# Performance work log

Measured on AMD Instinct MI355X. Metric: run time of the kernel, lower is better.

## Reference

```python
import jax, jax.numpy as jnp
import numpy as np

H = 256      # hidden_units
NB = 2       # num_blocks
NH = 4       # num_heads
E = 8        # num_experts
K = 2        # top_k
L = 200      # maxlen
B = 128      # batch
ITEM = 100000
USER = 50000


def _ln(x, w, b, eps):
    m = x.mean(-1, keepdims=True)
    v = ((x - m) ** 2).mean(-1, keepdims=True)
    return (x - m) / jnp.sqrt(v + eps) * w + b


def setup_inputs() -> dict:
    key = jax.random.key(0)
    ks = iter(jax.random.split(key, 48))

    def n(shape, s=0.02):
        return jax.random.normal(next(ks), shape, jnp.float32) * s

    item_emb = n((ITEM + 1, H)).at[0].set(0.0)   # padding_idx=0
    pos_emb = n((L + 1, H)).at[0].set(0.0)
    user_emb = n((USER + 1, H)).at[0].set(0.0)
    return dict(
        user_ids=jax.random.randint(next(ks), (B,), 1, USER + 1),
        log_seqs=jax.random.randint(next(ks), (B, L), 0, ITEM + 1),
        item_ids=jax.random.randint(next(ks), (B,), 1, ITEM + 1),
        item_emb=item_emb, pos_emb=pos_emb, user_emb=user_emb,
        ln1_w=jnp.ones((NB, H)), ln1_b=jnp.zeros((NB, H)),
        inproj_w=n((NB, 3 * H, H)), inproj_b=jnp.zeros((NB, 3 * H)),
        outproj_w=n((NB, H, H)), outproj_b=jnp.zeros((NB, H)),
        ln2_w=jnp.ones((NB, H)), ln2_b=jnp.zeros((NB, H)),
        gate_w=n((NB, E, H)), gate_b=jnp.zeros((NB, E)),
        e_w1=n((NB, E, H, H)), e_b1=jnp.zeros((NB, E, H)),
        e_w2=n((NB, E, H, H)), e_b2=jnp.zeros((NB, E, H)),
        moeln_w=jnp.ones((NB, H)), moeln_b=jnp.zeros((NB, H)),
        lastln_w=jnp.ones((H,)), lastln_b=jnp.zeros((H,)),
    )


def reference(user_ids, log_seqs, item_ids, item_emb, pos_emb, user_emb,
              ln1_w, ln1_b, inproj_w, inproj_b, outproj_w, outproj_b,
              ln2_w, ln2_b, gate_w, gate_b, e_w1, e_b1, e_w2, e_b2,
              moeln_w, moeln_b, lastln_w, lastln_b):
    hd = H // NH
    # embeddings (padding id 0 -> zero rows)
    x = item_emb[log_seqs] * jnp.sqrt(jnp.float32(H))          # [B,L,H]
    poss = jnp.arange(1, L + 1)[None, :] * (log_seqs != 0)      # 0 where padded
    x = x + pos_emb[poss]
    causal = jnp.tril(jnp.ones((L, L), bool))

    for i in range(NB):
        # pre-LN query, raw x as key/value (matches original)
        q_in = _ln(x, ln1_w[i], ln1_b[i], 1e-8)
        wq, wk, wv = jnp.split(inproj_w[i], 3, axis=0)
        bq, bk, bv = jnp.split(inproj_b[i], 3)
        q = (q_in @ wq.T + bq).reshape(B, L, NH, hd)
        k = (x @ wk.T + bk).reshape(B, L, NH, hd)
        v = (x @ wv.T + bv).reshape(B, L, NH, hd)
        s = jnp.einsum('bqnd,bknd->bnqk', q, k) / jnp.sqrt(jnp.float32(hd))
        s = jnp.where(causal, s, -jnp.inf)
        a = jax.nn.softmax(s, axis=-1)
        ctx = jnp.einsum('bnqk,bknd->bqnd', a, v).reshape(B, L, H)
        mha = ctx @ outproj_w[i].T + outproj_b[i]
        x = q_in + mha
        x = _ln(x, ln2_w[i], ln2_b[i], 1e-8)

        # SparseMoE: top-k gate, all-expert dense compute, masked combine
        gl = jnp.einsum('bsh,eh->bse', x, gate_w[i]) + gate_b[i]
        w, idx = jax.lax.top_k(gl, K)
        w = jax.nn.softmax(w, axis=-1)
        comb = (jax.nn.one_hot(idx, E) * w[..., None]).sum(-2)   # [B,L,E]
        h = jax.nn.relu(jnp.einsum('bsh,ehd->besd', x, e_w1[i])
                        + e_b1[i][None, :, None, :])              # [B,E,L,H]
        y = jnp.einsum('besd,edh->besh', h, e_w2[i]) + e_b2[i][None, :, None, :]
        moe = jnp.einsum('bse,besh->bsh', comb, y)
        x = _ln(x + moe, moeln_w[i], moeln_b[i], 1e-5)

    x = _ln(x, lastln_w, lastln_b, 1e-8)
    final = x[:, -1, :] + user_emb[user_ids]
    return (final * item_emb[item_ids]).sum(-1)   # [B] logits
```

## Files before the change

### kernel.cpp

```cpp
#include <hip/hip_runtime.h>
#include <math.h>

#define H 256
#define NHEAD 4
#define HD 64
#define NEXP 8
#define SEQL 200
#define BATCH 128
#define NF (BATCH*SEQL)
#define KT 64
#define QT 64
#define QW 8

typedef __bf16 bf16x8 __attribute__((ext_vector_type(8)));
typedef float  f32x4  __attribute__((ext_vector_type(4)));

__device__ __forceinline__ void split8(const float* __restrict__ p, bf16x8& hi, bf16x8& lo, bool valid) {
    if (valid) {
        float4 a = *(const float4*)p;
        float4 b = *(const float4*)(p + 4);
        float x[8] = {a.x,a.y,a.z,a.w,b.x,b.y,b.z,b.w};
        #pragma unroll
        for (int j = 0; j < 8; ++j) {
            __bf16 h = (__bf16)x[j];
            hi[j] = h;
            lo[j] = (__bf16)(x[j] - (float)h);
        }
    } else {
        #pragma unroll
        for (int j = 0; j < 8; ++j) { hi[j] = (__bf16)0.f; lo[j] = (__bf16)0.f; }
    }
}

#define MFMA3(AH,AL,BH,BL,ACC) \
    ACC = __builtin_amdgcn_mfma_f32_16x16x32_bf16(AH, BH, ACC, 0, 0, 0); \
    ACC = __builtin_amdgcn_mfma_f32_16x16x32_bf16(AH, BL, ACC, 0, 0, 0); \
    ACC = __builtin_amdgcn_mfma_f32_16x16x32_bf16(AL, BH, ACC, 0, 0, 0);

__device__ __forceinline__ float blk_sum256(float v, float* s4) {
    #pragma unroll
    for (int o = 32; o > 0; o >>= 1) v += __shfl_xor(v, o, 64);
    __syncthreads();
    if ((threadIdx.x & 63) == 0) s4[threadIdx.x >> 6] = v;
    __syncthreads();
    return s4[0] + s4[1] + s4[2] + s4[3];
}

__global__ __launch_bounds__(256) void split_plain(
    const float* __restrict__ in, __bf16* __restrict__ hi, __bf16* __restrict__ lo, int n)
{
    for (int i = blockIdx.x * 256 + threadIdx.x; i < n; i += gridDim.x * 256) {
        float x = in[i];
        __bf16 h = (__bf16)x;
        hi[i] = h;
        lo[i] = (__bf16)(x - (float)h);
    }
}

__global__ __launch_bounds__(256) void split_trans(
    const float* __restrict__ in, __bf16* __restrict__ hi, __bf16* __restrict__ lo, int nmats)
{
    int n = nmats * H * H;
    for (int i = blockIdx.x * 256 + threadIdx.x; i < n; i += gridDim.x * 256) {
        int m = i / (H*H), rem = i % (H*H);
        int nn = rem / H, k = rem % H;
        float x = in[(size_t)m*H*H + (size_t)k*H + nn];
        __bf16 h = (__bf16)x;
        hi[i] = h;
        lo[i] = (__bf16)(x - (float)h);
    }
}

__global__ __launch_bounds__(256) void embed_ln_kernel(
    const int* __restrict__ seqs, const float* __restrict__ item_emb,
    const float* __restrict__ pos_emb, float* __restrict__ x,
    float* __restrict__ xln, const float* __restrict__ w, const float* __restrict__ b)
{
    __shared__ float s4[4];
    int n = blockIdx.x, t = threadIdx.x;
    int id = seqs[n];
    int pos = (id != 0) ? (n % SEQL) + 1 : 0;
    float v = item_emb[(size_t)id*H + t] * 16.0f + pos_emb[(size_t)pos*H + t];
    x[(size_t)n*H + t] = v;
    float mean = blk_sum256(v, s4) * (1.f/H);
    float d = v - mean;
    float var = blk_sum256(d*d, s4) * (1.f/H);
    xln[(size_t)n*H + t] = d * rsqrtf(var + 1e-8f) * w[t] + b[t];
}

__global__ __launch_bounds__(256) void ln_kernel(
    const float* __restrict__ in, const float* __restrict__ res,
    float* __restrict__ out, const float* __restrict__ w, const float* __restrict__ b,
    float eps, int base, int step)
{
    __shared__ float s4[4];
    int r = blockIdx.x, t = threadIdx.x;
    float v = in[(size_t)(base + r*step)*H + t];
    if (res) v += res[(size_t)r*H + t];
    float mean = blk_sum256(v, s4) * (1.f/H);
    float d = v - mean;
    float var = blk_sum256(d*d, s4) * (1.f/H);
    out[(size_t)r*H + t] = d * rsqrtf(var + eps) * w[t] + b[t];
}

__global__ __launch_bounds__(256) void ln2_gate_kernel(
    const float* __restrict__ in, const float* __restrict__ res,
    float* __restrict__ out, const float* __restrict__ w, const float* __restrict__ b,
    const float* __restrict__ gw, const float* __restrict__ gb,
    int* __restrict__ top_idx, float* __restrict__ top_w)
{
    __shared__ float s4[4];
    __shared__ float xs[H];
    __shared__ float gl[NEXP];
    int n = blockIdx.x, t = threadIdx.x;
    float v = in[(size_t)n*H + t] + res[(size_t)n*H + t];
    float mean = blk_sum256(v, s4) * (1.f/H);
    float d = v - mean;
    float var = blk_sum256(d*d, s4) * (1.f/H);
    float r = d * rsqrtf(var + 1e-8f) * w[t] + b[t];
    out[(size_t)n*H + t] = r;
    xs[t] = r;
    __syncthreads();
    int wv = t >> 6, lane = t & 63;
    float xv[4];
    #pragma unroll
    for (int c = 0; c < 4; ++c) xv[c] = xs[lane + (c<<6)];
    #pragma unroll
    for (int s = 0; s < 2; ++s) {
        int e = wv*2 + s;
        float acc = 0.f;
        #pragma unroll
        for (int c = 0; c < 4; ++c) acc += xv[c] * gw[(size_t)e*H + lane + (c<<6)];
        #pragma unroll
        for (int o = 32; o > 0; o >>= 1) acc += __shfl_xor(acc, o, 64);
        if (lane == 0) gl[e] = acc + gb[e];
    }
    __syncthreads();
    if (t == 0) {
        int i0 = 0;
        for (int e = 1; e < NEXP; ++e) if (gl[e] > gl[i0]) i0 = e;
        int i1 = -1;
        for (int e = 0; e < NEXP; ++e) { if (e == i0) continue; if (i1 < 0 || gl[e] > gl[i1]) i1 = e; }
        float e1 = expf(gl[i1] - gl[i0]);
        float w0 = 1.f / (1.f + e1);
        top_idx[n*2+0] = i0; top_idx[n*2+1] = i1;
        top_w[n*2+0] = w0;  top_w[n*2+1] = 1.f - w0;
    }
}

__global__ __launch_bounds__(256) void moe_ln_kernel(
    const float* __restrict__ x, const float* __restrict__ ybuf,
    const int* __restrict__ tok_pair, const float* __restrict__ top_w,
    float* __restrict__ out, const float* __restrict__ w, const float* __restrict__ b,
    float eps)
{
    __shared__ float s4[4];
    int r = blockIdx.x, t = threadIdx.x;
    int p0 = tok_pair[r*2], p1 = tok_pair[r*2+1];
    float v = x[(size_t)r*H + t]
            + top_w[r*2+0] * ybuf[(size_t)p0*H + t]
            + top_w[r*2+1] * ybuf[(size_t)p1*H + t];
    float mean = blk_sum256(v, s4) * (1.f/H);
    float d = v - mean;
    float var = blk_sum256(d*d, s4) * (1.f/H);
    out[(size_t)r*H + t] = d * rsqrtf(var + eps) * w[t] + b[t];
}

__global__ __launch_bounds__(256) void gemm_nt(
    const float* __restrict__ A, const float* __restrict__ W,
    const float* __restrict__ bias, float* __restrict__ out, int nrows)
{
    __shared__ float As[16][68];
    __shared__ float Ws[16][68];
    int r0 = blockIdx.x * 64;
    if (r0 >= nrows) return;
    int c0 = blockIdx.y * 64;
    int tid = threadIdx.x;
    int tx = tid & 15, ty = tid >> 4;
    int lrow = tid >> 2, lkg = (tid & 3) << 2;
    float acc[4][4] = {};
    for (int kk = 0; kk < H; kk += 16) {
        float4 av = make_float4(0.f,0.f,0.f,0.f);
        int gr = r0 + lrow;
        if (gr < nrows) av = *(const float4*)(A + (size_t)gr*H + kk + lkg);
        As[lkg+0][lrow]=av.x; As[lkg+1][lrow]=av.y; As[lkg+2][lrow]=av.z; As[lkg+3][lrow]=av.w;
        float4 wv = *(const float4*)(W + (size_t)(c0+lrow)*H + kk + lkg);
        Ws[lkg+0][lrow]=wv.x; Ws[lkg+1][lrow]=wv.y; Ws[lkg+2][lrow]=wv.z; Ws[lkg+3][lrow]=wv.w;
        __syncthreads();
        #pragma unroll
        for (int k = 0; k < 16; ++k) {
            float4 a = *(const float4*)&As[k][ty<<2];
            float4 bv = *(const float4*)&Ws[k][tx<<2];
            float aa[4] = {a.x,a.y,a.z,a.w};
            float bb[4] = {bv.x,bv.y,bv.z,bv.w};
            #pragma unroll
            for (int ii = 0; ii < 4; ++ii)
                #pragma unroll
                for (int jj = 0; jj < 4; ++jj)
                    acc[ii][jj] += aa[ii] * bb[jj];
        }
        __syncthreads();
    }
    #pragma unroll
    for (int ii = 0; ii < 4; ++ii) {
        int gr = r0 + (ty<<2) + ii;
        if (gr < nrows) {
            #pragma unroll
            for (int jj = 0; jj < 4; ++jj) {
                int gc = c0 + (tx<<2) + jj;
                out[(size_t)gr*H + gc] = acc[ii][jj] + bias[gc];
            }
        }
    }
}

template<int GATHER, int RELU>
__device__ __forceinline__ void mfma64_body(
    const float* __restrict__ A, const __bf16* __restrict__ Whi, const __bf16* __restrict__ Wlo,
    const float* __restrict__ bias, float* __restrict__ out, int nrows,
    const int* __restrict__ pair_tok)
{
    int r0 = blockIdx.x * 64;
    if (r0 >= nrows) return;
    int tid = threadIdx.x;
    int wid = tid >> 6, lane = tid & 63;
    int wm = wid >> 1, wn = wid & 1;
    int rbase = r0 + wm*32;
    int lr = lane & 15, lk = (lane >> 4) << 3;
    f32x4 acc[4][2][2] = {};
    int ar0 = rbase + lr, ar1 = ar0 + 16;
    bool v0 = ar0 < nrows, v1 = ar1 < nrows;
    int ga0 = ar0, ga1 = ar1;
    if (GATHER) { ga0 = v0 ? pair_tok[ar0] : 0; ga1 = v1 ? pair_tok[ar1] : 0; }
    const float* ap0 = A + (size_t)(v0 ? ga0 : 0)*H + lk;
    const float* ap1 = A + (size_t)(v1 ? ga1 : 0)*H + lk;
    size_t woff = (size_t)(wn*32 + lr)*H + lk;
    #pragma unroll
    for (int kk = 0; kk < H; kk += 32) {
        bf16x8 ah0, al0, ah1, al1;
        split8(ap0 + kk, ah0, al0, v0);
        split8(ap1 + kk, ah1, al1, v1);
        #pragma unroll
        for (int ct = 0; ct < 4; ++ct) {
            size_t wo = woff + (size_t)ct*64*H + kk;
            bf16x8 bh0 = *(const bf16x8*)(Whi + wo);
            bf16x8 bl0 = *(const bf16x8*)(Wlo + wo);
            bf16x8 bh1 = *(const bf16x8*)(Whi + wo + (size_t)16*H);
            bf16x8 bl1 = *(const bf16x8*)(Wlo + wo + (size_t)16*H);
            MFMA3(ah0, al0, bh0, bl0, acc[ct][0][0]);
            MFMA3(ah0, al0, bh1, bl1, acc[ct][0][1]);
            MFMA3(ah1, al1, bh0, bl0, acc[ct][1][0]);
            MFMA3(ah1, al1, bh1, bl1, acc[ct][1][1]);
        }
    }
    int lro = (lane >> 4) << 2;
    #pragma unroll
    for (int ct = 0; ct < 4; ++ct)
        #pragma unroll
        for (int mi = 0; mi < 2; ++mi)
            #pragma unroll
            for (int ni = 0; ni < 2; ++ni)
                #pragma unroll
                for (int j = 0; j < 4; ++j) {
                    int row = rbase + mi*16 + lro + j;
                    int col = ct*64 + wn*32 + ni*16 + lr;
                    if (row < nrows) {
                        float o = acc[ct][mi][ni][j] + bias[col];
                        if (RELU) o = fmaxf(o, 0.f);
                        out[(size_t)row*H + col] = o;
                    }
                }
}

__global__ __launch_bounds__(256) void mfma_z(
    const float* __restrict__ A0, const float* __restrict__ A1,
    const __bf16* __restrict__ Whi, const __bf16* __restrict__ Wlo,
    const float* __restrict__ biasbase, float* __restrict__ outbase, int nrows)
{
    int z = blockIdx.z;
    const float* A = (z == 0) ? A0 : A1;
    mfma64_body<0,0>(A, Whi + (size_t)z*H*H, Wlo + (size_t)z*H*H,
                     biasbase + (size_t)z*H, outbase + (size_t)z*NF*H, nrows, nullptr);
}

__global__ __launch_bounds__(256) void mfma_moe1(
    const float* __restrict__ X, const __bf16* __restrict__ Whi, const __bf16* __restrict__ Wlo,
    const float* __restrict__ b1base, const int* __restrict__ pair_tok,
    const int* __restrict__ offsets, const int* __restrict__ counts,
    float* __restrict__ hbuf)
{
    int e = blockIdx.z;
    int cnt = counts[e], off = offsets[e];
    mfma64_body<1,1>(X, Whi + (size_t)e*H*H, Wlo + (size_t)e*H*H,
                     b1base + (size_t)e*H, hbuf + (size_t)off*H, cnt, pair_tok + off);
}

__global__ __launch_bounds__(256) void mfma_moe2(
    const float* __restrict__ Hbuf, const __bf16* __restrict__ Whi, const __bf16* __restrict__ Wlo,
    const float* __restrict__ b2base, const int* __restrict__ offsets,
    const int* __restrict__ counts, float* __restrict__ ybuf)
{
    int e = blockIdx.z;
    int cnt = counts[e], off = offsets[e];
    mfma64_body<0,0>(Hbuf + (size_t)off*H, Whi + (size_t)e*H*H, Wlo + (size_t)e*H*H,
                     b2base + (size_t)e*H, ybuf + (size_t)off*H, cnt, nullptr);
}

__global__ __launch_bounds__(512) void attn_kernel(
    const float* __restrict__ qbuf, const float* __restrict__ kbuf,
    const float* __restrict__ vbuf, float* __restrict__ ctx, int nq)
{
    __shared__ float kv[KT*(HD+4)];
    __shared__ float qs[QT][HD+4];
    __shared__ float ps[QT][KT+4];
    int b = blockIdx.x, h = blockIdx.y, z = blockIdx.z;
    int qbase = z * QT;
    int nqt = nq - qbase;
    if (nqt <= 0) return;
    if (nqt > QT) nqt = QT;
    int tid = threadIdx.x, w = tid >> 6, lane = tid & 63;
    int off = SEQL - nq;
    for (int i = tid; i < QT*(HD/4); i += 512) {
        int row = i >> 4, c4 = (i & 15) << 2;
        float4 qv = make_float4(0.f,0.f,0.f,0.f);
        if (row < nqt) qv = *(const float4*)(qbuf + (size_t)(b*nq + qbase + row)*H + h*HD + c4);
        *(float4*)&qs[row][c4] = qv;
    }
    float m[QW], l[QW], acc[QW];
    #pragma unroll
    for (int i = 0; i < QW; ++i) { m[i] = -3e30f; l[i] = 0.f; acc[i] = 0.f; }
    int wq0 = w * QW;
    int wqn = nqt - wq0; if (wqn > QW) wqn = QW;
    int wmaxpos = qbase + wq0 + (wqn > 0 ? wqn - 1 : 0) + off;
    int ntiles = (qbase + nqt - 1 + off) / KT + 1;
    int q_sub = lane >> 3, kq = lane & 7;
    for (int t = 0; t < ntiles; ++t) {
        int kbase = t * KT;
        bool active = (wqn > 0) && (kbase <= wmaxpos);
        __syncthreads();
        for (int i = tid; i < KT*(HD/4); i += 512) {
            int row = i >> 4, c4 = (i & 15) << 2;
            int key = kbase + row;
            float4 kvv = make_float4(0.f,0.f,0.f,0.f);
            if (key < SEQL) kvv = *(const float4*)(kbuf + (size_t)(b*SEQL + key)*H + h*HD + c4);
            *(float4*)&kv[row*(HD+4) + c4] = kvv;
        }
        __syncthreads();
        if (active) {
            float s[QW];
            #pragma unroll
            for (int qi = 0; qi < QW; ++qi) s[qi] = 0.f;
            #pragma unroll 4
            for (int d4 = 0; d4 < HD; d4 += 4) {
                float4 k4 = *(const float4*)&kv[lane*(HD+4) + d4];
                #pragma unroll
                for (int qi = 0; qi < QW; ++qi) {
                    float4 q4 = *(const float4*)&qs[wq0+qi][d4];
                    s[qi] += k4.x*q4.x + k4.y*q4.y + k4.z*q4.z + k4.w*q4.w;
                }
            }
            #pragma unroll
            for (int qi = 0; qi < QW; ++qi) {
                if (qi < wqn) {
                    int qpos = qbase + wq0 + qi + off;
                    bool valid = (kbase + lane) <= qpos;
                    ps[wq0+qi][lane] = valid ? s[qi]*0.125f : -3e30f;
                }
            }
        }
        __syncthreads();
        {
            int key = kbase + lane;
            bool kval = key < SEQL;
            const float* vp = vbuf + (size_t)(b*SEQL + (kval ? key : 0))*H + h*HD;
            #pragma unroll
            for (int it = 0; it < 2; ++it) {
                int c4 = ((it << 3) + w) << 2;
                float4 vv = make_float4(0.f,0.f,0.f,0.f);
                if (kval) vv = *(const float4*)(vp + c4);
                kv[(c4+0)*(KT+4) + lane] = vv.x;
                kv[(c4+1)*(KT+4) + lane] = vv.y;
                kv[(c4+2)*(KT+4) + lane] = vv.z;
                kv[(c4+3)*(KT+4) + lane] = vv.w;
            }
        }
        __syncthreads();
        if (active) {
            float mq = m[0];
            #pragma unroll
            for (int i = 1; i < QW; ++i) if (q_sub == i) mq = m[i];
            const float2* pr = (const float2*)&ps[wq0+q_sub][kq*8];
            float2 a0 = pr[0], a1 = pr[1], a2 = pr[2], a3 = pr[3];
            float mloc = fmaxf(fmaxf(fmaxf(a0.x,a0.y), fmaxf(a1.x,a1.y)),
                               fmaxf(fmaxf(a2.x,a2.y), fmaxf(a3.x,a3.y)));
            float tm = mloc;
            #pragma unroll
            for (int o = 1; o < 8; o <<= 1) tm = fmaxf(tm, __shfl_xor(tm, o, 64));
            float mn = fmaxf(mq, tm);
            float p0 = expf(a0.x-mn), p1 = expf(a0.y-mn), p2 = expf(a1.x-mn), p3 = expf(a1.y-mn);
            float p4 = expf(a2.x-mn), p5 = expf(a2.y-mn), p6 = expf(a3.x-mn), p7 = expf(a3.y-mn);
            float psum = ((p0+p1)+(p2+p3)) + ((p4+p5)+(p6+p7));
            #pragma unroll
            for (int o = 1; o < 8; o <<= 1) psum += __shfl_xor(psum, o, 64);
            float2* pw = (float2*)&ps[wq0+q_sub][kq*8];
            pw[0] = make_float2(p0,p1); pw[1] = make_float2(p2,p3);
            pw[2] = make_float2(p4,p5); pw[3] = make_float2(p6,p7);
            #pragma unroll
            for (int qi = 0; qi < QW; ++qi) {
                float tmv = __shfl(tm, qi*8, 64);
                float psv = __shfl(psum, qi*8, 64);
                if (qi < wqn) {
                    float mn2 = fmaxf(m[qi], tmv);
                    float scl = expf(m[qi] - mn2);
                    l[qi] = l[qi]*scl + psv;
                    acc[qi] *= scl;
                    m[qi] = mn2;
                }
            }
            #pragma unroll 4
            for (int k4 = 0; k4 < KT; k4 += 4) {
                float4 v4 = *(const float4*)&kv[lane*(KT+4) + k4];
                #pragma unroll
                for (int qi = 0; qi < QW; ++qi) {
                    if (qi < wqn) {
                        float4 p4v = *(const float4*)&ps[wq0+qi][k4];
                        acc[qi] += p4v.x*v4.x + p4v.y*v4.y + p4v.z*v4.z + p4v.w*v4.w;
                    }
                }
            }
        }
    }
    #pragma unroll
    for (int qi = 0; qi < QW; ++qi) {
        if (qi < wqn) {
            ctx[(size_t)(b*nq + qbase + wq0 + qi)*H + h*HD + lane] = acc[qi] / l[qi];
        }
    }
}

__global__ __launch_bounds__(256) void count_kernel(
    const int* __restrict__ top_idx, int* __restrict__ counts, int nrows)
{
    __shared__ int hist[NEXP];
    int tid = threadIdx.x;
    if (tid < NEXP) hist[tid] = 0;
    __syncthreads();
    int n = blockIdx.x * 256 + tid;
    if (n < nrows) {
        atomicAdd(&hist[top_idx[n*2+0]], 1);
        atomicAdd(&hist[top_idx[n*2+1]], 1);
    }
    __syncthreads();
    if (tid < NEXP && hist[tid] > 0) atomicAdd(&counts[tid], hist[tid]);
}

__global__ void scan_kernel(const int* __restrict__ counts, int* __restrict__ offsets,
                            int* __restrict__ cursor)
{
    int s = 0;
    for (int e = 0; e < NEXP; ++e) { offsets[e] = s; cursor[e] = s; s += counts[e]; }
}

__global__ __launch_bounds__(256) void scatter_kernel(
    const int* __restrict__ top_idx,
    int* __restrict__ cursor, int* __restrict__ pair_tok, int* __restrict__ tok_pair, int nrows)
{
    __shared__ int lcnt[NEXP];
    __shared__ int lbase[NEXP];
    int tid = threadIdx.x;
    if (tid < NEXP) lcnt[tid] = 0;
    __syncthreads();
    int n = blockIdx.x * 256 + tid;
    int e0 = 0, e1 = 0, p0 = 0, p1 = 0;
    bool act = n < nrows;
    if (act) {
        e0 = top_idx[n*2+0]; e1 = top_idx[n*2+1];
        p0 = atomicAdd(&lcnt[e0], 1);
        p1 = atomicAdd(&lcnt[e1], 1);
    }
    __syncthreads();
    if (tid < NEXP) lbase[tid] = (lcnt[tid] > 0) ? atomicAdd(&cursor[tid], lcnt[tid]) : 0;
    __syncthreads();
    if (act) {
        int q0 = lbase[e0] + p0, q1 = lbase[e1] + p1;
        pair_tok[q0] = n; pair_tok[q1] = n;
        tok_pair[n*2+0] = q0; tok_pair[n*2+1] = q1;
    }
}

__global__ __launch_bounds__(256) void moe_gemm1(
    const float* __restrict__ X, const float* __restrict__ W1base,
    const float* __restrict__ b1base, const int* __restrict__ pair_tok,
    const int* __restrict__ offsets, const int* __restrict__ counts,
    float* __restrict__ hbuf)
{
    int e = blockIdx.z;
    int cnt = counts[e];
    int r0 = blockIdx.x * 64;
    if (r0 >= cnt) return;
    int off = offsets[e];
    int c0 = blockIdx.y * 64;
    const float* W = W1base + (size_t)e * H * H;
    const float* bias = b1base + (size_t)e * H;
    __shared__ float As[16][68];
    __shared__ float Bs[16][68];
    int tid = threadIdx.x, tx = tid & 15, ty = tid >> 4;
    int lrow = tid >> 2, lkg = (tid & 3) << 2;
    float acc[4][4] = {};
    for (int kk = 0; kk < H; kk += 16) {
        float4 av = make_float4(0.f,0.f,0.f,0.f);
        int pr = r0 + lrow;
        if (pr < cnt) {
            int tok = pair_tok[off + pr];
            av = *(const float4*)(X + (size_t)tok*H + kk + lkg);
        }
        As[lkg+0][lrow]=av.x; As[lkg+1][lrow]=av.y; As[lkg+2][lrow]=av.z; As[lkg+3][lrow]=av.w;
        float4 wv = *(const float4*)(W + (size_t)(kk+ty)*H + c0 + (tx<<2));
        *(float4*)&Bs[ty][tx<<2] = wv;
        __syncthreads();
        #pragma unroll
        for (int k = 0; k < 16; ++k) {
            float4 a = *(const float4*)&As[k][ty<<2];
            float4 bv = *(const float4*)&Bs[k][tx<<2];
            float aa[4] = {a.x,a.y,a.z,a.w};
            float bb[4] = {bv.x,bv.y,bv.z,bv.w};
            #pragma unroll
            for (int ii = 0; ii < 4; ++ii)
                #pragma unroll
                for (int jj = 0; jj < 4; ++jj)
                    acc[ii][jj] += aa[ii] * bb[jj];
        }
        __syncthreads();
    }
    #pragma unroll
    for (int ii = 0; ii < 4; ++ii) {
        int pr = r0 + (ty<<2) + ii;
        if (pr < cnt) {
            #pragma unroll
            for (int jj = 0; jj < 4; ++jj) {
                int gc = c0 + (tx<<2) + jj;
                hbuf[(size_t)(off+pr)*H + gc] = fmaxf(acc[ii][jj] + bias[gc], 0.f);
            }
        }
    }
}

__global__ __launch_bounds__(256) void moe_gemm2(
    const float* __restrict__ Hbuf, const float* __restrict__ W2base,
    const float* __restrict__ b2base, const int* __restrict__ offsets,
    const int* __restrict__ counts, float* __restrict__ ybuf)
{
    int e = blockIdx.z;
    int cnt = counts[e];
    int r0 = blockIdx.x * 64;
    if (r0 >= cnt) return;
    int off = offsets[e];
    int c0 = blockIdx.y * 64;
    const float* W = W2base + (size_t)e * H * H;
    const float* bias = b2base + (size_t)e * H;
    __shared__ float As[16][68];
    __shared__ float Bs[16][68];
    int tid = threadIdx.x, tx = tid & 15, ty = tid >> 4;
    int lrow = tid >> 2, lkg = (tid & 3) << 2;
    float acc[4][4] = {};
    for (int kk = 0; kk < H; kk += 16) {
        float4 av = make_float4(0.f,0.f,0.f,0.f);
        int pr = r0 + lrow;
        if (pr < cnt) av = *(const float4*)(Hbuf + (size_t)(off+pr)*H + kk + lkg);
        As[lkg+0][lrow]=av.x; As[lkg+1][lrow]=av.y; As[lkg+2][lrow]=av.z; As[lkg+3][lrow]=av.w;
        float4 wv = *(const float4*)(W + (size_t)(kk+ty)*H + c0 + (tx<<2));
        *(float4*)&Bs[ty][tx<<2] = wv;
        __syncthreads();
        #pragma unroll
        for (int k = 0; k < 16; ++k) {
            float4 a = *(const float4*)&As[k][ty<<2];
            float4 bv = *(const float4*)&Bs[k][tx<<2];
            float aa[4] = {a.x,a.y,a.z,a.w};
            float bb[4] = {bv.x,bv.y,bv.z,bv.w};
            #pragma unroll
            for (int ii = 0; ii < 4; ++ii)
                #pragma unroll
                for (int jj = 0; jj < 4; ++jj)
                    acc[ii][jj] += aa[ii] * bb[jj];
        }
        __syncthreads();
    }
    #pragma unroll
    for (int ii = 0; ii < 4; ++ii) {
        int pr = r0 + (ty<<2) + ii;
        if (pr < cnt) {
            #pragma unroll
            for (int jj = 0; jj < 4; ++jj) {
                int gc = c0 + (tx<<2) + jj;
                ybuf[(size_t)(off+pr)*H + gc] = acc[ii][jj] + bias[gc];
            }
        }
    }
}

__global__ void zero_kernel(float* __restrict__ p, int n) {
    int i = blockIdx.x * 256 + threadIdx.x;
    if (i < n) p[i] = 0.f;
}

__global__ __launch_bounds__(256) void final_kernel(
    const float* __restrict__ xf, const float* __restrict__ lnw, const float* __restrict__ lnb,
    const float* __restrict__ user_emb, const float* __restrict__ item_emb,
    const int* __restrict__ user_ids, const int* __restrict__ item_ids, float* __restrict__ out)
{
    __shared__ float s4[4];
    int bb = blockIdx.x, t = threadIdx.x;
    float v = xf[(size_t)bb*H + t];
    float mean = blk_sum256(v, s4) * (1.f/H);
    float d = v - mean;
    float var = blk_sum256(d*d, s4) * (1.f/H);
    float lnv = d * rsqrtf(var + 1e-8f) * lnw[t] + lnb[t];
    float fin = lnv + user_emb[(size_t)user_ids[bb]*H + t];
    float prod = fin * item_emb[(size_t)item_ids[bb]*H + t];
    float tot = blk_sum256(prod, s4);
    if (t == 0) out[bb] = tot;
}

extern "C" void kernel_launch(void* const* d_in, const int* in_sizes, int n_in,
                              void* d_out, int out_size, void* d_ws, size_t ws_size,
                              hipStream_t stream)
{
    (void)in_sizes; (void)n_in; (void)out_size; (void)ws_size;
    const int*   user_ids  = (const int*)d_in[0];
    const int*   log_seqs  = (const int*)d_in[1];
    const int*   item_ids  = (const int*)d_in[2];
    const float* item_emb  = (const float*)d_in[3];
    const float* pos_emb   = (const float*)d_in[4];
    const float* user_emb  = (const float*)d_in[5];
    const float* ln1_w     = (const float*)d_in[6];
    const float* ln1_b     = (const float*)d_in[7];
    const float* inproj_w  = (const float*)d_in[8];
    const float* inproj_b  = (const float*)d_in[9];
    const float* outproj_w = (const float*)d_in[10];
    const float* outproj_b = (const float*)d_in[11];
    const float* ln2_w     = (const float*)d_in[12];
    const float* ln2_b     = (const float*)d_in[13];
    const float* gate_w    = (const float*)d_in[14];
    const float* gate_b    = (const float*)d_in[15];
    const float* e_w1      = (const float*)d_in[16];
    const float* e_b1      = (const float*)d_in[17];
    const float* e_w2      = (const float*)d_in[18];
    const float* e_b2      = (const float*)d_in[19];
    const float* moeln_w   = (const float*)d_in[20];
    const float* moeln_b   = (const float*)d_in[21];
    const float* lastln_w  = (const float*)d_in[22];
    const float* lastln_b  = (const float*)d_in[23];

    float* ws = (float*)d_ws;
    const size_t NFH = (size_t)NF * H;
    float* buf0 = ws;
    float* buf1 = buf0 + NFH;
    float* buf2 = buf1 + NFH;
    float* buf3 = buf2 + NFH;
    float* buf4 = buf3 + NFH;
    float* s0   = buf4 + NFH;
    float* s1   = s0 + (size_t)BATCH*H;
    float* s2   = s1 + (size_t)BATCH*H;
    float* s3   = s2 + (size_t)BATCH*H;
    float* s6   = s3 + (size_t)BATCH*H;
    float* s4   = s6 + (size_t)BATCH*H;
    float* s5   = s4 + (size_t)2*BATCH*H;
    float* top_w   = s5 + (size_t)2*BATCH*H;
    int*   top_idx = (int*)(top_w + (size_t)NF*2);
    int*   pair_tok= top_idx + (size_t)NF*2;
    int*   tok_pair= pair_tok + (size_t)NF*2;
    int*   counts  = tok_pair + (size_t)NF*2;
    int*   offsets = counts + NEXP;
    int*   cursor  = offsets + NEXP;
    const size_t W_IP = (size_t)2*3*H*H;
    const size_t W_OP = (size_t)2*H*H;
    const size_t W_E  = (size_t)2*NEXP*H*H;
    __bf16* ip_hi = (__bf16*)(cursor + 64);
    __bf16* ip_lo = ip_hi + W_IP;
    __bf16* op_hi = ip_lo + W_IP;
    __bf16* op_lo = op_hi + W_OP;
    __bf16* e1_hi = op_lo + W_OP;
    __bf16* e1_lo = e1_hi + W_E;
    __bf16* e2_hi = e1_lo + W_E;
    __bf16* e2_lo = e2_hi + W_E;

    dim3 blk(256);
    dim3 ablk(512);
    dim3 m64z3(NF/64, 1, 3);
    dim3 m64z2(NF/64, 1, 2);
    dim3 m64z1(NF/64, 1, 1);
    dim3 m64e(NF/64, 1, NEXP);
    dim3 gsmall((BATCH+63)/64, H/64);
    dim3 msmall((BATCH+63)/64, H/64, NEXP);

    split_plain<<<512, blk, 0, stream>>>(inproj_w,  ip_hi, ip_lo, (int)W_IP);
    split_plain<<<256, blk, 0, stream>>>(outproj_w, op_hi, op_lo, (int)W_OP);
    split_trans<<<1024, blk, 0, stream>>>(e_w1, e1_hi, e1_lo, 2*NEXP);
    split_trans<<<1024, blk, 0, stream>>>(e_w2, e2_hi, e2_lo, 2*NEXP);

    {
        const int i = 0;
        const float* bq = inproj_b + (size_t)i*3*H;
        embed_ln_kernel<<<NF, blk, 0, stream>>>(log_seqs, item_emb, pos_emb, buf0, buf1,
                                                ln1_w + i*H, ln1_b + i*H);
        mfma_z<<<m64z3, blk, 0, stream>>>(buf1, buf0, ip_hi, ip_lo, bq, buf2, NF);
        attn_kernel<<<dim3(BATCH, NHEAD, (SEQL+QT-1)/QT), ablk, 0, stream>>>(buf2, buf3, buf4, buf2, SEQL);
        mfma_z<<<m64z1, blk, 0, stream>>>(buf2, buf2, op_hi, op_lo, outproj_b, buf3, NF);
        ln2_gate_kernel<<<NF, blk, 0, stream>>>(buf1, buf3, buf0, ln2_w + i*H, ln2_b + i*H,
                                                gate_w + (size_t)i*NEXP*H, gate_b + i*NEXP,
                                                top_idx, top_w);
        zero_kernel<<<1, 32, 0, stream>>>((float*)counts, NEXP);
        count_kernel<<<(NF+255)/256, blk, 0, stream>>>(top_idx, counts, NF);
        scan_kernel<<<1, 1, 0, stream>>>(counts, offsets, cursor);
        scatter_kernel<<<(NF+255)/256, blk, 0, stream>>>(top_idx, cursor, pair_tok, tok_pair, NF);
        mfma_moe1<<<m64e, blk, 0, stream>>>(buf0, e1_hi, e1_lo, e_b1 + (size_t)i*NEXP*H,
                                            pair_tok, offsets, counts, buf3);
        mfma_moe2<<<m64e, blk, 0, stream>>>(buf3, e2_hi, e2_lo, e_b2 + (size_t)i*NEXP*H,
                                            offsets, counts, buf1);
        moe_ln_kernel<<<NF, blk, 0, stream>>>(buf0, buf1, tok_pair, top_w, buf3,
                                              moeln_w + i*H, moeln_b + i*H, 1e-5f);
    }

    {
        const int i = 1;
        const float* Wq = inproj_w + (size_t)i*3*H*H;
        const float* bq = inproj_b + (size_t)i*3*H;
        float* X = buf3;
        ln_kernel<<<BATCH, blk, 0, stream>>>(X, nullptr, s0, ln1_w + i*H, ln1_b + i*H, 1e-8f, SEQL-1, SEQL);
        gemm_nt<<<gsmall, blk, 0, stream>>>(s0, Wq, bq, s1, BATCH);
        mfma_z<<<m64z2, blk, 0, stream>>>(X, X, ip_hi + (size_t)3*H*H + (size_t)H*H,
                                          ip_lo + (size_t)3*H*H + (size_t)H*H, bq + H, buf0, NF);
        attn_kernel<<<dim3(BATCH, NHEAD, 1), ablk, 0, stream>>>(s1, buf0, buf1, s2, 1);
        gemm_nt<<<gsmall, blk, 0, stream>>>(s2, outproj_w + (size_t)i*H*H, outproj_b + i*H, s3, BATCH);
        ln2_gate_kernel<<<BATCH, blk, 0, stream>>>(s0, s3, s2, ln2_w + i*H, ln2_b + i*H,
                                                   gate_w + (size_t)i*NEXP*H, gate_b + i*NEXP,
                                                   top_idx, top_w);
        zero_kernel<<<1, 32, 0, stream>>>((float*)counts, NEXP);
        count_kernel<<<1, blk, 0, stream>>>(top_idx, counts, BATCH);
        scan_kernel<<<1, 1, 0, stream>>>(counts, offsets, cursor);
        scatter_kernel<<<1, blk, 0, stream>>>(top_idx, cursor, pair_tok, tok_pair, BATCH);
        moe_gemm1<<<msmall, blk, 0, stream>>>(s2, e_w1 + (size_t)i*NEXP*H*H, e_b1 + (size_t)i*NEXP*H,
                                              pair_tok, offsets, counts, s4);
        moe_gemm2<<<msmall, blk, 0, stream>>>(s4, e_w2 + (size_t)i*NEXP*H*H, e_b2 + (size_t)i*NEXP*H,
                                              offsets, counts, s5);
        moe_ln_kernel<<<BATCH, blk, 0, stream>>>(s2, s5, tok_pair, top_w, s6,
                                                 moeln_w + i*H, moeln_b + i*H, 1e-5f);
    }

    final_kernel<<<BATCH, blk, 0, stream>>>(s6, lastln_w, lastln_b, user_emb, item_emb,
                                            user_ids, item_ids, (float*)d_out);
}
```

Before: 892.2 us.

## Fold K and V projections into query for last-block single-row attention

For the second block, only the last query row is needed. Instead of projecting the full sequence to K and V with a large GEMM, the query is multiplied through Wk (and bk folded into a per-head scalar), scores are computed directly against raw X, softmax-weighted X is averaged, and only the averaged rows are projected through Wv. This removes the NF×2H K/V projection GEMM and its memory traffic, at the cost of three small fp32 kernels and reliance on softmax weights summing to one for the bias term.

```diff
diff --git a/kernel.cpp b/kernel.cpp
--- a/kernel.cpp
+++ b/kernel.cpp
@@ -210,6 +210,126 @@
                 int gc = c0 + (tx<<2) + jj;
                 out[(size_t)gr*H + gc] = acc[ii][jj] + bias[gc];
             }
+        }
+    }
+}
+
+__global__ __launch_bounds__(256) void qfold_kernel(
+    const float* __restrict__ q, const float* __restrict__ Wk, const float* __restrict__ bk,
+    float* __restrict__ qt, float* __restrict__ qbk)
+{
+    __shared__ float qs[H];
+    int b = blockIdx.x, t = threadIdx.x;
+    qs[t] = q[(size_t)b*H + t];
+    __syncthreads();
+    #pragma unroll
+    for (int h = 0; h < NHEAD; ++h) {
+        float acc = 0.f;
+        #pragma unroll 8
+        for (int d = 0; d < HD; ++d)
+            acc += qs[h*HD + d] * Wk[(size_t)(h*HD + d)*H + t];
+        qt[((size_t)h*BATCH + b)*H + t] = acc;
+    }
+    if (t < NHEAD) {
+        float acc = 0.f;
+        for (int d = 0; d < HD; ++d) acc += qs[t*HD + d] * bk[t*HD + d];
+        qbk[b*NHEAD + t] = acc;
+    }
+}
+
+__global__ __launch_bounds__(256) void attn1_kernel(
+    const float* __restrict__ qt, const float* __restrict__ qbk,
+    const float* __restrict__ X, float* __restrict__ xbar)
+{
+    __shared__ float qts[NHEAD][H];
+    __shared__ float as[NHEAD][SEQL];
+    int b = blockIdx.x;
+    int tid = threadIdx.x, w = tid >> 6, lane = tid & 63;
+    for (int i = tid; i < NHEAD*H; i += 256) {
+        int h = i >> 8, j = i & (H-1);
+        qts[h][j] = qt[((size_t)h*BATCH + b)*H + j];
+    }
+    __syncthreads();
+    float qb = qbk[b*NHEAD + w];
+    const float4 qv = *(const float4*)&qts[w][lane<<2];
+    for (int key = 0; key < SEQL; ++key) {
+        const float4 xv = *(const float4*)(X + (size_t)(b*SEQL + key)*H + (lane<<2));
+        float p = xv.x*qv.x + xv.y*qv.y + xv.z*qv.z + xv.w*qv.w;
+        #pragma unroll
+        for (int o = 32; o > 0; o >>= 1) p += __shfl_xor(p, o, 64);
+        if (lane == 0) as[w][key] = (p + qb) * 0.125f;
+    }
+    __syncthreads();
+    float m = -3e30f;
+    for (int key = lane; key < SEQL; key += 64) m = fmaxf(m, as[w][key]);
+    #pragma unroll
+    for (int o = 32; o > 0; o >>= 1) m = fmaxf(m, __shfl_xor(m, o, 64));
+    float sum = 0.f;
+    for (int key = lane; key < SEQL; key += 64) {
+        float e = expf(as[w][key] - m);
+        sum += e;
+    }
+    #pragma unroll
+    for (int o = 32; o > 0; o >>= 1) sum += __shfl_xor(sum, o, 64);
+    float inv = 1.f / sum;
+    __syncthreads();
+    for (int key = lane; key < SEQL; key += 64)
+        as[w][key] = expf(as[w][key] - m) * inv;
+    __syncthreads();
+    float4 acc = make_float4(0.f,0.f,0.f,0.f);
+    for (int key = 0; key < SEQL; ++key) {
+        float a = as[w][key];
+        const float4 xv = *(const float4*)(X + (size_t)(b*SEQL + key)*H + (lane<<2));
+        acc.x += a*xv.x; acc.y += a*xv.y; acc.z += a*xv.z; acc.w += a*xv.w;
+    }
+    *(float4*)(xbar + ((size_t)w*BATCH + b)*H + (lane<<2)) = acc;
+}
+
+__global__ __launch_bounds__(256) void ctx_gemm(
+    const float* __restrict__ xbar, const float* __restrict__ Wv,
+    const float* __restrict__ bv, float* __restrict__ out)
+{
+    int h = blockIdx.z;
+    const float* A = xbar + (size_t)h*BATCH*H;
+    const float* W = Wv + (size_t)h*HD*H;
+    const float* bias = bv + h*HD;
+    float* O = out + h*HD;
+    __shared__ float As[16][68];
+    __shared__ float Ws[16][68];
+    int r0 = blockIdx.x * 64;
+    int tid = threadIdx.x;
+    int tx = tid & 15, ty = tid >> 4;
+    int lrow = tid >> 2, lkg = (tid & 3) << 2;
+    float acc[4][4] = {};
+    for (int kk = 0; kk < H; kk += 16) {
+        float4 av = *(const float4*)(A + (size_t)(r0 + lrow)*H + kk + lkg);
+        As[lkg+0][lrow]=av.x; As[lkg+1][lrow]=av.y; As[lkg+2][lrow]=av.z; As[lkg+3][lrow]=av.w;
+        float4 wv;
+        if (lrow < HD) wv = *(const float4*)(W + (size_t)lrow*H + kk + lkg);
+        else wv = make_float4(0.f,0.f,0.f,0.f);
+        Ws[lkg+0][lrow]=wv.x; Ws[lkg+1][lrow]=wv.y; Ws[lkg+2][lrow]=wv.z; Ws[lkg+3][lrow]=wv.w;
+        __syncthreads();
+        #pragma unroll
+        for (int k = 0; k < 16; ++k) {
+            float4 a = *(const float4*)&As[k][ty<<2];
+            float4 bv4 = *(const float4*)&Ws[k][tx<<2];
+            float aa[4] = {a.x,a.y,a.z,a.w};
+            float bb[4] = {bv4.x,bv4.y,bv4.z,bv4.w};
+            #pragma unroll
+            for (int ii = 0; ii < 4; ++ii)
+                #pragma unroll
+                for (int jj = 0; jj < 4; ++jj)
+                    acc[ii][jj] += aa[ii] * bb[jj];
+        }
+        __syncthreads();
+    }
+    #pragma unroll
+    for (int ii = 0; ii < 4; ++ii) {
+        int gr = r0 + (ty<<2) + ii;
+        #pragma unroll
+        for (int jj = 0; jj < 4; ++jj) {
+            int gc = (tx<<2) + jj;
+            if (gc < HD) O[(size_t)gr*H + gc] = acc[ii][jj] + bias[gc];
         }
     }
 }
@@ -683,11 +803,13 @@
     __bf16* e1_lo = e1_hi + W_E;
     __bf16* e2_hi = e1_lo + W_E;
     __bf16* e2_lo = e2_hi + W_E;
+    float* qt   = buf4;
+    float* xbar = qt + (size_t)NHEAD*BATCH*H;
+    float* qbk  = xbar + (size_t)NHEAD*BATCH*H;
 
     dim3 blk(256);
     dim3 ablk(512);
     dim3 m64z3(NF/64, 1, 3);
-    dim3 m64z2(NF/64, 1, 2);
     dim3 m64z1(NF/64, 1, 1);
     dim3 m64e(NF/64, 1, NEXP);
     dim3 gsmall((BATCH+63)/64, H/64);
@@ -724,13 +846,15 @@
     {
         const int i = 1;
         const float* Wq = inproj_w + (size_t)i*3*H*H;
+        const float* Wk = Wq + (size_t)H*H;
+        const float* Wv = Wk + (size_t)H*H;
         const float* bq = inproj_b + (size_t)i*3*H;
         float* X = buf3;
         ln_kernel<<<BATCH, blk, 0, stream>>>(X, nullptr, s0, ln1_w + i*H, ln1_b + i*H, 1e-8f, SEQL-1, SEQL);
         gemm_nt<<<gsmall, blk, 0, stream>>>(s0, Wq, bq, s1, BATCH);
-        mfma_z<<<m64z2, blk, 0, stream>>>(X, X, ip_hi + (size_t)3*H*H + (size_t)H*H,
-                                          ip_lo + (size_t)3*H*H + (size_t)H*H, bq + H, buf0, NF);
-        attn_kernel<<<dim3(BATCH, NHEAD, 1), ablk, 0, stream>>>(s1, buf0, buf1, s2, 1);
+        qfold_kernel<<<BATCH, blk, 0, stream>>>(s1, Wk, bq + H, qt, qbk);
+        attn1_kernel<<<BATCH, blk, 0, stream>>>(qt, qbk, X, xbar);
+        ctx_gemm<<<dim3(BATCH/64, 1, NHEAD), blk, 0, stream>>>(xbar, Wv, bq + 2*H, s2);
         gemm_nt<<<gsmall, blk, 0, stream>>>(s2, outproj_w + (size_t)i*H*H, outproj_b + i*H, s3, BATCH);
         ln2_gate_kernel<<<BATCH, blk, 0, stream>>>(s0, s3, s2, ln2_w + i*H, ln2_b + i*H,
                                                    gate_w + (size_t)i*NEXP*H, gate_b + i*NEXP,
```

Result: no change. 891.6 us (-0.1%).

## Fuse last-block attention via query-folded keys and merge weight-split kernels

Applied to the files above, without the earlier changes.

The second transformer block only needs the last position, so the separate LN, Q projection, full-sequence K/V projection, attention, out-projection and gate kernels are replaced by one per-batch kernel. It folds Wk into the query (q·Wk) and applies Wv after the attention-weighted sum of raw x, which removes the large K/V GEMM over all tokens. The four weight hi/lo split kernels are also merged into one launch. The fused kernel does fp32 scalar work per batch with only 128 blocks, and the reordered arithmetic may change rounding slightly.

```diff
diff --git a/kernel.cpp b/kernel.cpp
--- a/kernel.cpp
+++ b/kernel.cpp
@@ -46,28 +46,36 @@
     return s4[0] + s4[1] + s4[2] + s4[3];
 }
 
-__global__ __launch_bounds__(256) void split_plain(
-    const float* __restrict__ in, __bf16* __restrict__ hi, __bf16* __restrict__ lo, int n)
-{
-    for (int i = blockIdx.x * 256 + threadIdx.x; i < n; i += gridDim.x * 256) {
-        float x = in[i];
+__global__ __launch_bounds__(256) void split_all(
+    const float* __restrict__ ipw, const float* __restrict__ opw,
+    const float* __restrict__ ew1, const float* __restrict__ ew2,
+    __bf16* __restrict__ ip_hi, __bf16* __restrict__ ip_lo,
+    __bf16* __restrict__ op_hi, __bf16* __restrict__ op_lo,
+    __bf16* __restrict__ e1_hi, __bf16* __restrict__ e1_lo,
+    __bf16* __restrict__ e2_hi, __bf16* __restrict__ e2_lo)
+{
+    const int N_IP = 2*3*H*H;
+    const int N_OP = 2*H*H;
+    const int N_E  = 2*NEXP*H*H;
+    const int TOT  = N_IP + N_OP + 2*N_E;
+    for (int i = blockIdx.x*256 + threadIdx.x; i < TOT; i += gridDim.x*256) {
+        float x; __bf16 *hi, *lo; int idx;
+        if (i < N_IP) {
+            idx = i; x = ipw[idx]; hi = ip_hi; lo = ip_lo;
+        } else if (i < N_IP + N_OP) {
+            idx = i - N_IP; x = opw[idx]; hi = op_hi; lo = op_lo;
+        } else if (i < N_IP + N_OP + N_E) {
+            idx = i - N_IP - N_OP;
+            int m = idx/(H*H), rem = idx%(H*H); int nn = rem/H, k = rem%H;
+            x = ew1[(size_t)m*H*H + (size_t)k*H + nn]; hi = e1_hi; lo = e1_lo;
+        } else {
+            idx = i - N_IP - N_OP - N_E;
+            int m = idx/(H*H), rem = idx%(H*H); int nn = rem/H, k = rem%H;
+            x = ew2[(size_t)m*H*H + (size_t)k*H + nn]; hi = e2_hi; lo = e2_lo;
+        }
         __bf16 h = (__bf16)x;
-        hi[i] = h;
-        lo[i] = (__bf16)(x - (float)h);
-    }
-}
-
-__global__ __launch_bounds__(256) void split_trans(
-    const float* __restrict__ in, __bf16* __restrict__ hi, __bf16* __restrict__ lo, int nmats)
-{
-    int n = nmats * H * H;
-    for (int i = blockIdx.x * 256 + threadIdx.x; i < n; i += gridDim.x * 256) {
-        int m = i / (H*H), rem = i % (H*H);
-        int nn = rem / H, k = rem % H;
-        float x = in[(size_t)m*H*H + (size_t)k*H + nn];
-        __bf16 h = (__bf16)x;
-        hi[i] = h;
-        lo[i] = (__bf16)(x - (float)h);
+        hi[idx] = h;
+        lo[idx] = (__bf16)(x - (float)h);
     }
 }
 
@@ -86,21 +94,6 @@
     float d = v - mean;
     float var = blk_sum256(d*d, s4) * (1.f/H);
     xln[(size_t)n*H + t] = d * rsqrtf(var + 1e-8f) * w[t] + b[t];
-}
-
-__global__ __launch_bounds__(256) void ln_kernel(
-    const float* __restrict__ in, const float* __restrict__ res,
-    float* __restrict__ out, const float* __restrict__ w, const float* __restrict__ b,
-    float eps, int base, int step)
-{
-    __shared__ float s4[4];
-    int r = blockIdx.x, t = threadIdx.x;
-    float v = in[(size_t)(base + r*step)*H + t];
-    if (res) v += res[(size_t)r*H + t];
-    float mean = blk_sum256(v, s4) * (1.f/H);
-    float d = v - mean;
-    float var = blk_sum256(d*d, s4) * (1.f/H);
-    out[(size_t)r*H + t] = d * rsqrtf(var + eps) * w[t] + b[t];
 }
 
 __global__ __launch_bounds__(256) void ln2_gate_kernel(
@@ -166,51 +159,148 @@
     out[(size_t)r*H + t] = d * rsqrtf(var + eps) * w[t] + b[t];
 }
 
-__global__ __launch_bounds__(256) void gemm_nt(
-    const float* __restrict__ A, const float* __restrict__ W,
-    const float* __restrict__ bias, float* __restrict__ out, int nrows)
-{
-    __shared__ float As[16][68];
-    __shared__ float Ws[16][68];
-    int r0 = blockIdx.x * 64;
-    if (r0 >= nrows) return;
-    int c0 = blockIdx.y * 64;
-    int tid = threadIdx.x;
-    int tx = tid & 15, ty = tid >> 4;
-    int lrow = tid >> 2, lkg = (tid & 3) << 2;
-    float acc[4][4] = {};
-    for (int kk = 0; kk < H; kk += 16) {
-        float4 av = make_float4(0.f,0.f,0.f,0.f);
-        int gr = r0 + lrow;
-        if (gr < nrows) av = *(const float4*)(A + (size_t)gr*H + kk + lkg);
-        As[lkg+0][lrow]=av.x; As[lkg+1][lrow]=av.y; As[lkg+2][lrow]=av.z; As[lkg+3][lrow]=av.w;
-        float4 wv = *(const float4*)(W + (size_t)(c0+lrow)*H + kk + lkg);
-        Ws[lkg+0][lrow]=wv.x; Ws[lkg+1][lrow]=wv.y; Ws[lkg+2][lrow]=wv.z; Ws[lkg+3][lrow]=wv.w;
-        __syncthreads();
-        #pragma unroll
-        for (int k = 0; k < 16; ++k) {
-            float4 a = *(const float4*)&As[k][ty<<2];
-            float4 bv = *(const float4*)&Ws[k][tx<<2];
-            float aa[4] = {a.x,a.y,a.z,a.w};
-            float bb[4] = {bv.x,bv.y,bv.z,bv.w};
-            #pragma unroll
-            for (int ii = 0; ii < 4; ++ii)
-                #pragma unroll
-                for (int jj = 0; jj < 4; ++jj)
-                    acc[ii][jj] += aa[ii] * bb[jj];
-        }
-        __syncthreads();
-    }
-    #pragma unroll
-    for (int ii = 0; ii < 4; ++ii) {
-        int gr = r0 + (ty<<2) + ii;
-        if (gr < nrows) {
-            #pragma unroll
-            for (int jj = 0; jj < 4; ++jj) {
-                int gc = c0 + (tx<<2) + jj;
-                out[(size_t)gr*H + gc] = acc[ii][jj] + bias[gc];
-            }
-        }
+__global__ __launch_bounds__(256) void block1_fused(
+    const float* __restrict__ X,
+    const float* __restrict__ ln1w, const float* __restrict__ ln1b,
+    const float* __restrict__ Wq, const float* __restrict__ bq,
+    const float* __restrict__ Wk, const float* __restrict__ bk,
+    const float* __restrict__ Wv, const float* __restrict__ bv,
+    const float* __restrict__ Wo, const float* __restrict__ bo,
+    const float* __restrict__ ln2w, const float* __restrict__ ln2b,
+    const float* __restrict__ gw, const float* __restrict__ gb,
+    float* __restrict__ s2_out, int* __restrict__ top_idx, float* __restrict__ top_w,
+    int* __restrict__ counts)
+{
+    __shared__ float s4r[4];
+    __shared__ float s0s[H];
+    __shared__ float qs[H];
+    __shared__ float qts[NHEAD][H];
+    __shared__ float qbks[NHEAD];
+    __shared__ float as_[NHEAD][SEQL];
+    __shared__ float xbars[NHEAD][H];
+    __shared__ float ctxs[H];
+    __shared__ float gl[NEXP];
+    int b = blockIdx.x, t = threadIdx.x;
+    int w = t >> 6, lane = t & 63;
+    float v = X[(size_t)(b*SEQL + SEQL-1)*H + t];
+    float mean = blk_sum256(v, s4r) * (1.f/H);
+    float d = v - mean;
+    float var = blk_sum256(d*d, s4r) * (1.f/H);
+    float s0v = d * rsqrtf(var + 1e-8f) * ln1w[t] + ln1b[t];
+    s0s[t] = s0v;
+    __syncthreads();
+    {
+        const float* wr = Wq + (size_t)t*H;
+        float acc = 0.f;
+        for (int dd = 0; dd < H; dd += 4) {
+            float4 w4 = *(const float4*)(wr + dd);
+            acc += s0s[dd]*w4.x + s0s[dd+1]*w4.y + s0s[dd+2]*w4.z + s0s[dd+3]*w4.w;
+        }
+        qs[t] = acc + bq[t];
+    }
+    __syncthreads();
+    #pragma unroll
+    for (int h = 0; h < NHEAD; ++h) {
+        float acc = 0.f;
+        #pragma unroll 8
+        for (int dd = 0; dd < HD; ++dd)
+            acc += qs[h*HD + dd] * Wk[(size_t)(h*HD + dd)*H + t];
+        qts[h][t] = acc;
+    }
+    if (t < NHEAD) {
+        float acc = 0.f;
+        for (int dd = 0; dd < HD; ++dd) acc += qs[t*HD + dd] * bk[t*HD + dd];
+        qbks[t] = acc;
+    }
+    __syncthreads();
+    {
+        float qb = qbks[w];
+        const float4 qv = *(const float4*)&qts[w][lane<<2];
+        for (int key = 0; key < SEQL; ++key) {
+            const float4 xv = *(const float4*)(X + (size_t)(b*SEQL + key)*H + (lane<<2));
+            float p = xv.x*qv.x + xv.y*qv.y + xv.z*qv.z + xv.w*qv.w;
+            #pragma unroll
+            for (int o = 32; o > 0; o >>= 1) p += __shfl_xor(p, o, 64);
+            if (lane == 0) as_[w][key] = (p + qb) * 0.125f;
+        }
+        __syncthreads();
+        float m = -3e30f;
+        for (int key = lane; key < SEQL; key += 64) m = fmaxf(m, as_[w][key]);
+        #pragma unroll
+        for (int o = 32; o > 0; o >>= 1) m = fmaxf(m, __shfl_xor(m, o, 64));
+        float sum = 0.f;
+        for (int key = lane; key < SEQL; key += 64) sum += expf(as_[w][key] - m);
+        #pragma unroll
+        for (int o = 32; o > 0; o >>= 1) sum += __shfl_xor(sum, o, 64);
+        float inv = 1.f / sum;
+        __syncthreads();
+        for (int key = lane; key < SEQL; key += 64)
+            as_[w][key] = expf(as_[w][key] - m) * inv;
+        __syncthreads();
+        float4 acc4 = make_float4(0.f,0.f,0.f,0.f);
+        for (int key = 0; key < SEQL; ++key) {
+            float a = as_[w][key];
+            const float4 xv = *(const float4*)(X + (size_t)(b*SEQL + key)*H + (lane<<2));
+            acc4.x += a*xv.x; acc4.y += a*xv.y; acc4.z += a*xv.z; acc4.w += a*xv.w;
+        }
+        *(float4*)&xbars[w][lane<<2] = acc4;
+    }
+    __syncthreads();
+    {
+        int h = t >> 6;
+        const float* wr = Wv + (size_t)t*H;
+        float acc = 0.f;
+        for (int dd = 0; dd < H; dd += 4) {
+            float4 w4 = *(const float4*)(wr + dd);
+            acc += xbars[h][dd]*w4.x + xbars[h][dd+1]*w4.y + xbars[h][dd+2]*w4.z + xbars[h][dd+3]*w4.w;
+        }
+        ctxs[t] = acc + bv[t];
+    }
+    __syncthreads();
+    float mha;
+    {
+        const float* wr = Wo + (size_t)t*H;
+        float acc = 0.f;
+        for (int dd = 0; dd < H; dd += 4) {
+            float4 w4 = *(const float4*)(wr + dd);
+            acc += ctxs[dd]*w4.x + ctxs[dd+1]*w4.y + ctxs[dd+2]*w4.z + ctxs[dd+3]*w4.w;
+        }
+        mha = acc + bo[t];
+    }
+    float v2 = s0s[t] + mha;
+    mean = blk_sum256(v2, s4r) * (1.f/H);
+    d = v2 - mean;
+    var = blk_sum256(d*d, s4r) * (1.f/H);
+    float r = d * rsqrtf(var + 1e-8f) * ln2w[t] + ln2b[t];
+    s2_out[(size_t)b*H + t] = r;
+    __syncthreads();
+    s0s[t] = r;
+    __syncthreads();
+    float xv[4];
+    #pragma unroll
+    for (int c = 0; c < 4; ++c) xv[c] = s0s[lane + (c<<6)];
+    #pragma unroll
+    for (int s = 0; s < 2; ++s) {
+        int e = w*2 + s;
+        float acc = 0.f;
+        #pragma unroll
+        for (int c = 0; c < 4; ++c) acc += xv[c] * gw[(size_t)e*H + lane + (c<<6)];
+        #pragma unroll
+        for (int o = 32; o > 0; o >>= 1) acc += __shfl_xor(acc, o, 64);
+        if (lane == 0) gl[e] = acc + gb[e];
+    }
+    __syncthreads();
+    if (t == 0) {
+        int i0 = 0;
+        for (int e = 1; e < NEXP; ++e) if (gl[e] > gl[i0]) i0 = e;
+        int i1 = -1;
+        for (int e = 0; e < NEXP; ++e) { if (e == i0) continue; if (i1 < 0 || gl[e] > gl[i1]) i1 = e; }
+        float e1 = expf(gl[i1] - gl[i0]);
+        float w0 = 1.f / (1.f + e1);
+        top_idx[b*2+0] = i0; top_idx[b*2+1] = i1;
+        top_w[b*2+0] = w0;  top_w[b*2+1] = 1.f - w0;
+        atomicAdd(&counts[i0], 1);
+        atomicAdd(&counts[i1], 1);
     }
 }
 
@@ -687,16 +777,13 @@
     dim3 blk(256);
     dim3 ablk(512);
     dim3 m64z3(NF/64, 1, 3);
-    dim3 m64z2(NF/64, 1, 2);
     dim3 m64z1(NF/64, 1, 1);
     dim3 m64e(NF/64, 1, NEXP);
-    dim3 gsmall((BATCH+63)/64, H/64);
     dim3 msmall((BATCH+63)/64, H/64, NEXP);
 
-    split_plain<<<512, blk, 0, stream>>>(inproj_w,  ip_hi, ip_lo, (int)W_IP);
-    split_plain<<<256, blk, 0, stream>>>(outproj_w, op_hi, op_lo, (int)W_OP);
-    split_trans<<<1024, blk, 0, stream>>>(e_w1, e1_hi, e1_lo, 2*NEXP);
-    split_trans<<<1024, blk, 0, stream>>>(e_w2, e2_hi, e2_lo, 2*NEXP);
+    split_all<<<2048, blk, 0, stream>>>(inproj_w, outproj_w, e_w1, e_w2,
+                                        ip_hi, ip_lo, op_hi, op_lo,
+                                        e1_hi, e1_lo, e2_hi, e2_lo);
 
     {
         const int i = 0;
@@ -724,19 +811,18 @@
     {
         const int i = 1;
         const float* Wq = inproj_w + (size_t)i*3*H*H;
+        const float* Wk = Wq + (size_t)H*H;
+        const float* Wv = Wk + (size_t)H*H;
         const float* bq = inproj_b + (size_t)i*3*H;
         float* X = buf3;
-        ln_kernel<<<BATCH, blk, 0, stream>>>(X, nullptr, s0, ln1_w + i*H, ln1_b + i*H, 1e-8f, SEQL-1, SEQL);
-        gemm_nt<<<gsmall, blk, 0, stream>>>(s0, Wq, bq, s1, BATCH);
-        mfma_z<<<m64z2, blk, 0, stream>>>(X, X, ip_hi + (size_t)3*H*H + (size_t)H*H,
-                                          ip_lo + (size_t)3*H*H + (size_t)H*H, bq + H, buf0, NF);
-        attn_kernel<<<dim3(BATCH, NHEAD, 1), ablk, 0, stream>>>(s1, buf0, buf1, s2, 1);
-        gemm_nt<<<gsmall, blk, 0, stream>>>(s2, outproj_w + (size_t)i*H*H, outproj_b + i*H, s3, BATCH);
-        ln2_gate_kernel<<<BATCH, blk, 0, stream>>>(s0, s3, s2, ln2_w + i*H, ln2_b + i*H,
-                                                   gate_w + (size_t)i*NEXP*H, gate_b + i*NEXP,
-                                                   top_idx, top_w);
         zero_kernel<<<1, 32, 0, stream>>>((float*)counts, NEXP);
-        count_kernel<<<1, blk, 0, stream>>>(top_idx, counts, BATCH);
+        block1_fused<<<BATCH, blk, 0, stream>>>(
+            X, ln1_w + i*H, ln1_b + i*H,
+            Wq, bq, Wk, bq + H, Wv, bq + 2*H,
+            outproj_w + (size_t)i*H*H, outproj_b + i*H,
+            ln2_w + i*H, ln2_b + i*H,
+            gate_w + (size_t)i*NEXP*H, gate_b + i*NEXP,
+            s2, top_idx, top_w, counts);
         scan_kernel<<<1, 1, 0, stream>>>(counts, offsets, cursor);
         scatter_kernel<<<1, blk, 0, stream>>>(top_idx, cursor, pair_tok, tok_pair, BATCH);
         moe_gemm1<<<msmall, blk, 0, stream>>>(s2, e_w1 + (size_t)i*NEXP*H*H, e_b1 + (size_t)i*NEXP*H,
```

Result: faster. 848.3 us (-4.9%).
